# Kernel tuning notes

Hardware: AMD Instinct MI355X
Metric: run time of the kernel (lower is better)

## Reference

```python
import math
import jax, jax.numpy as jnp
import numpy as np

L, T, F = 16, 524288, 2
N_MIN, N_MAX = 16, 2048
N_POINTS = 1_048_576

# 4 bilinear corner offsets, same order as the original module
VERT_OFFSETS = jnp.asarray([[0, 0], [0, 1], [1, 0], [1, 1]], dtype=jnp.int32)


def _smallest_prime_geq(n):
    def is_prime(m):
        if m < 2:
            return False
        for p in range(2, int(m ** 0.5) + 1):
            if m % p == 0:
                return False
        return True
    while not is_prime(n):
        n += 1
    return n

PRIME = _smallest_prime_geq(2 ** 17)  # second spatial hashing prime (first is 1)


def _grid_meta():
    # per-level resolution, hashed-vs-dense flag, and offsets into the flat table
    b = math.exp((math.log(N_MAX) - math.log(N_MIN)) / (L - 1))
    resolutions, hashed, offsets = [], [], [0]
    for i in range(L):
        res = int(N_MIN * b ** i)
        n_entries = (res + 1) ** 2
        h = n_entries > T
        if h:
            n_entries = T
        resolutions.append(res)
        hashed.append(h)
        offsets.append(offsets[-1] + n_entries)
    return resolutions, hashed, offsets


def setup_inputs() -> dict:
    key = jax.random.key(0)
    k1, k2 = jax.random.split(key)
    _, _, offsets = _grid_meta()
    uv = jax.random.uniform(k1, (N_POINTS, 2), jnp.float32)  # points in [0,1)^2
    latents = jax.random.uniform(k2, (offsets[-1], F), jnp.float32, -1e-4, 1e-4)
    return {"uv": uv, "latents": latents}


def _encode(uv, latents):
    resolutions, hashed, offsets = _grid_meta()
    encs = []
    for i in range(L):  # fixed small level loop (structurally distinct per level)
        res = resolutions[i]
        uv_scaled = uv * res                                   # [N, 2]
        uv_floored = jnp.floor(uv_scaled).astype(jnp.int32)    # [N, 2]
        vert_uv = uv_floored[:, None, :] + VERT_OFFSETS        # [N, 4, 2]
        if hashed[i]:
            idx = jnp.mod(
                jnp.bitwise_xor(vert_uv[..., 0] * 1, vert_uv[..., 1] * PRIME), T
            )                                                  # [N, 4]
        else:
            idx = vert_uv[..., 0] * res + vert_uv[..., 1]      # [N, 4]
        vert_latents = latents[idx + offsets[i]]               # [N, 4, F] gather
        # bilinear lerp weights, exactly as lerp_weights in the module
        pos_offset = uv_scaled[:, None, :] - vert_uv[:, 0:1, :]          # [N, 1->4, 2]
        widths = jnp.clip(1 - VERT_OFFSETS + (2 * VERT_OFFSETS - 1) * pos_offset, 0, 1)
        w = jnp.prod(widths, axis=-1)                          # [N, 4]
        encs.append((vert_latents * w[..., None]).sum(axis=-2))  # [N, F]
    # original: stack [L,N,F] -> transpose(1,0,2) -> reshape(N, L*F) == concat on -1
    return jnp.concatenate(encs, axis=-1)                      # [N, L*F]


def reference(uv, latents):
    return _encode(uv, latents)
```

## Files before the change

### kernel.cpp

```cpp
#include <hip/hip_runtime.h>
#include <math.h>

#define NLEVELS 16
#define NDENSE 12
#define NHASH 4
#define TBITS 19
#define TMASK ((1 << TBITS) - 1)

typedef float vfloat4 __attribute__((ext_vector_type(4)));

struct Meta {
    float resf[NLEVELS];
    int   resi[NLEVELS];
    int   off[NLEVELS];
    int   prime;
};

__global__ __launch_bounds__(256, 1) void hashgrid2d_kernel(
    const float2* __restrict__ uv,
    const float2* __restrict__ lat,
    float* __restrict__ out,
    Meta m, int n)
{
    int p = blockIdx.x * blockDim.x + threadIdx.x;
    if (p >= n) return;

    float2 u = uv[p];
    const float* latf = (const float*)lat;

    float4 da[NDENSE];
    float4 db[NDENSE];
    float2 hv[NHASH][4];

#pragma unroll
    for (int i = 0; i < NDENSE; ++i) {
        float sx = u.x * m.resf[i];
        float sy = u.y * m.resf[i];
        int x0 = (int)floorf(sx);
        int y0 = (int)floorf(sy);
        int base0 = m.off[i] + x0 * m.resi[i] + y0;
        int base1 = base0 + m.resi[i];
        __builtin_memcpy(&da[i], latf + 2 * (size_t)base0, 16);
        __builtin_memcpy(&db[i], latf + 2 * (size_t)base1, 16);
    }
#pragma unroll
    for (int h = 0; h < NHASH; ++h) {
        int i = NDENSE + h;
        float sx = u.x * m.resf[i];
        float sy = u.y * m.resf[i];
        int x0 = (int)floorf(sx);
        int y0 = (int)floorf(sy);
        int yp0 = y0 * m.prime;
        int yp1 = yp0 + m.prime;
        int x1  = x0 + 1;
        const float2* tbl = lat + m.off[i];
        hv[h][0] = tbl[(x0 ^ yp0) & TMASK];
        hv[h][1] = tbl[(x0 ^ yp1) & TMASK];
        hv[h][2] = tbl[(x1 ^ yp0) & TMASK];
        hv[h][3] = tbl[(x1 ^ yp1) & TMASK];
    }

    __builtin_amdgcn_sched_barrier(0);

    float o[2 * NLEVELS];
#pragma unroll
    for (int i = 0; i < NDENSE; ++i) {
        float sx = u.x * m.resf[i];
        float sy = u.y * m.resf[i];
        float fx = floorf(sx), fy = floorf(sy);
        float px = sx - fx,   py = sy - fy;
        float w00 = (1.0f - px) * (1.0f - py);
        float w01 = (1.0f - px) * py;
        float w10 = px * (1.0f - py);
        float w11 = px * py;
        o[2*i]   = w00 * da[i].x + w01 * da[i].z + w10 * db[i].x + w11 * db[i].z;
        o[2*i+1] = w00 * da[i].y + w01 * da[i].w + w10 * db[i].y + w11 * db[i].w;
    }
#pragma unroll
    for (int h = 0; h < NHASH; ++h) {
        int i = NDENSE + h;
        float sx = u.x * m.resf[i];
        float sy = u.y * m.resf[i];
        float fx = floorf(sx), fy = floorf(sy);
        float px = sx - fx,   py = sy - fy;
        float w00 = (1.0f - px) * (1.0f - py);
        float w01 = (1.0f - px) * py;
        float w10 = px * (1.0f - py);
        float w11 = px * py;
        o[2*i]   = w00 * hv[h][0].x + w01 * hv[h][1].x + w10 * hv[h][2].x + w11 * hv[h][3].x;
        o[2*i+1] = w00 * hv[h][0].y + w01 * hv[h][1].y + w10 * hv[h][2].y + w11 * hv[h][3].y;
    }

    vfloat4* op = (vfloat4*)(out + (size_t)p * (2 * NLEVELS));
#pragma unroll
    for (int j = 0; j < 8; ++j) {
        vfloat4 w;
        w.x = o[4 * j + 0];
        w.y = o[4 * j + 1];
        w.z = o[4 * j + 2];
        w.w = o[4 * j + 3];
        op[j] = w;
    }
}

static void compute_meta(Meta& m)
{
    const double b = exp((log(2048.0) - log(16.0)) / 15.0);
    int off = 0;
    const long long T = 1LL << TBITS;
    for (int i = 0; i < NLEVELS; ++i) {
        int res = (int)(16.0 * pow(b, (double)i));
        long long n_entries = (long long)(res + 1) * (long long)(res + 1);
        if (n_entries > T) n_entries = T;
        m.resf[i] = (float)res;
        m.resi[i] = res;
        m.off[i]  = off;
        off += (int)n_entries;
    }

    int pr = 1 << 17;
    for (;;) {
        bool isp = true;
        for (long long q = 2; q * q <= pr; ++q)
            if (pr % q == 0) { isp = false; break; }
        if (isp) break;
        ++pr;
    }
    m.prime = pr;
}

extern "C" void kernel_launch(void* const* d_in, const int* in_sizes, int n_in,
                              void* d_out, int out_size, void* d_ws, size_t ws_size,
                              hipStream_t stream)
{
    const float2* uv  = (const float2*)d_in[0];
    const float2* lat = (const float2*)d_in[1];
    float* out = (float*)d_out;

    int n = in_sizes[0] / 2;

    Meta m;
    compute_meta(m);

    const int block = 256;
    const int grid = (n + block - 1) / block;
    hashgrid2d_kernel<<<grid, block, 0, stream>>>(uv, lat, out, m, n);
}
```

Measured before the change: 338.2 us.

## Split hashed levels into per-level kernels writing workspace before dense assembly

Each of the four hashed levels is now handled by its own kernel launch, which gathers that level's four corners, interpolates them, and writes a float2 per point to workspace. A final kernel gathers the dense levels, reads the four precomputed hash results, and writes the output. The aim is to keep each 4 MB hash table's random-access footprint cache-resident during its own pass instead of all four competing at once. In exchange there are extra launches, extra workspace writes and reads, and uv is re-read five times. If the workspace is too small, the original monolithic kernel is kept as a fallback.

```diff
diff --git a/kernel.cpp b/kernel.cpp
--- a/kernel.cpp
+++ b/kernel.cpp
@@ -16,9 +16,40 @@
     int   prime;
 };
 
-__global__ __launch_bounds__(256, 1) void hashgrid2d_kernel(
+__global__ void hash_level_kernel(
     const float2* __restrict__ uv,
     const float2* __restrict__ lat,
+    float2* __restrict__ ws_out,
+    float resf, int off, int prime, int n)
+{
+    int p = blockIdx.x * blockDim.x + threadIdx.x;
+    if (p >= n) return;
+    float2 u = uv[p];
+    float sx = u.x * resf, sy = u.y * resf;
+    float fx = floorf(sx), fy = floorf(sy);
+    int x0 = (int)fx, y0 = (int)fy;
+    float px = sx - fx, py = sy - fy;
+    int yp0 = y0 * prime;
+    int yp1 = yp0 + prime;
+    const float2* tb = lat + off;
+    float2 c00 = tb[(x0 ^ yp0) & TMASK];
+    float2 c01 = tb[(x0 ^ yp1) & TMASK];
+    float2 c10 = tb[((x0 + 1) ^ yp0) & TMASK];
+    float2 c11 = tb[((x0 + 1) ^ yp1) & TMASK];
+    float w00 = (1.0f - px) * (1.0f - py);
+    float w01 = (1.0f - px) * py;
+    float w10 = px * (1.0f - py);
+    float w11 = px * py;
+    float2 r;
+    r.x = w00 * c00.x + w01 * c01.x + w10 * c10.x + w11 * c11.x;
+    r.y = w00 * c00.y + w01 * c01.y + w10 * c10.y + w11 * c11.y;
+    ws_out[p] = r;
+}
+
+__global__ __launch_bounds__(256, 1) void dense_assemble_kernel(
+    const float2* __restrict__ uv,
+    const float2* __restrict__ lat,
+    const float2* __restrict__ ws,
     float* __restrict__ out,
     Meta m, int n)
 {
@@ -30,7 +61,7 @@
 
     float4 da[NDENSE];
     float4 db[NDENSE];
-    float2 hv[NHASH][4];
+    float2 hres[NHASH];
 
 #pragma unroll
     for (int i = 0; i < NDENSE; ++i) {
@@ -44,21 +75,8 @@
         __builtin_memcpy(&db[i], latf + 2 * (size_t)base1, 16);
     }
 #pragma unroll
-    for (int h = 0; h < NHASH; ++h) {
-        int i = NDENSE + h;
-        float sx = u.x * m.resf[i];
-        float sy = u.y * m.resf[i];
-        int x0 = (int)floorf(sx);
-        int y0 = (int)floorf(sy);
-        int yp0 = y0 * m.prime;
-        int yp1 = yp0 + m.prime;
-        int x1  = x0 + 1;
-        const float2* tbl = lat + m.off[i];
-        hv[h][0] = tbl[(x0 ^ yp0) & TMASK];
-        hv[h][1] = tbl[(x0 ^ yp1) & TMASK];
-        hv[h][2] = tbl[(x1 ^ yp0) & TMASK];
-        hv[h][3] = tbl[(x1 ^ yp1) & TMASK];
-    }
+    for (int h = 0; h < NHASH; ++h)
+        hres[h] = ws[(size_t)h * n + p];
 
     __builtin_amdgcn_sched_barrier(0);
 
@@ -78,7 +96,62 @@
     }
 #pragma unroll
     for (int h = 0; h < NHASH; ++h) {
+        o[2*(NDENSE+h)]   = hres[h].x;
+        o[2*(NDENSE+h)+1] = hres[h].y;
+    }
+
+    vfloat4* op = (vfloat4*)(out + (size_t)p * (2 * NLEVELS));
+#pragma unroll
+    for (int j = 0; j < 8; ++j) {
+        vfloat4 w;
+        w.x = o[4*j+0]; w.y = o[4*j+1]; w.z = o[4*j+2]; w.w = o[4*j+3];
+        op[j] = w;
+    }
+}
+
+__global__ __launch_bounds__(256, 1) void hashgrid2d_mono_kernel(
+    const float2* __restrict__ uv,
+    const float2* __restrict__ lat,
+    float* __restrict__ out,
+    Meta m, int n)
+{
+    int p = blockIdx.x * blockDim.x + threadIdx.x;
+    if (p >= n) return;
+    float2 u = uv[p];
+    const float* latf = (const float*)lat;
+    float4 da[NDENSE];
+    float4 db[NDENSE];
+    float2 hv[NHASH][4];
+#pragma unroll
+    for (int i = 0; i < NDENSE; ++i) {
+        float sx = u.x * m.resf[i];
+        float sy = u.y * m.resf[i];
+        int x0 = (int)floorf(sx);
+        int y0 = (int)floorf(sy);
+        int base0 = m.off[i] + x0 * m.resi[i] + y0;
+        int base1 = base0 + m.resi[i];
+        __builtin_memcpy(&da[i], latf + 2 * (size_t)base0, 16);
+        __builtin_memcpy(&db[i], latf + 2 * (size_t)base1, 16);
+    }
+#pragma unroll
+    for (int h = 0; h < NHASH; ++h) {
         int i = NDENSE + h;
+        float sx = u.x * m.resf[i];
+        float sy = u.y * m.resf[i];
+        int x0 = (int)floorf(sx);
+        int y0 = (int)floorf(sy);
+        int yp0 = y0 * m.prime;
+        int yp1 = yp0 + m.prime;
+        const float2* tb = lat + m.off[i];
+        hv[h][0] = tb[(x0 ^ yp0) & TMASK];
+        hv[h][1] = tb[(x0 ^ yp1) & TMASK];
+        hv[h][2] = tb[((x0+1) ^ yp0) & TMASK];
+        hv[h][3] = tb[((x0+1) ^ yp1) & TMASK];
+    }
+    __builtin_amdgcn_sched_barrier(0);
+    float o[2 * NLEVELS];
+#pragma unroll
+    for (int i = 0; i < NDENSE; ++i) {
         float sx = u.x * m.resf[i];
         float sy = u.y * m.resf[i];
         float fx = floorf(sx), fy = floorf(sy);
@@ -87,18 +160,28 @@
         float w01 = (1.0f - px) * py;
         float w10 = px * (1.0f - py);
         float w11 = px * py;
-        o[2*i]   = w00 * hv[h][0].x + w01 * hv[h][1].x + w10 * hv[h][2].x + w11 * hv[h][3].x;
-        o[2*i+1] = w00 * hv[h][0].y + w01 * hv[h][1].y + w10 * hv[h][2].y + w11 * hv[h][3].y;
-    }
-
+        o[2*i]   = w00 * da[i].x + w01 * da[i].z + w10 * db[i].x + w11 * db[i].z;
+        o[2*i+1] = w00 * da[i].y + w01 * da[i].w + w10 * db[i].y + w11 * db[i].w;
+    }
+#pragma unroll
+    for (int h = 0; h < NHASH; ++h) {
+        int i = NDENSE + h;
+        float sx = u.x * m.resf[i];
+        float sy = u.y * m.resf[i];
+        float fx = floorf(sx), fy = floorf(sy);
+        float px = sx - fx,   py = sy - fy;
+        float w00 = (1.0f - px) * (1.0f - py);
+        float w01 = (1.0f - px) * py;
+        float w10 = px * (1.0f - py);
+        float w11 = px * py;
+        o[2*i]   = w00*hv[h][0].x + w01*hv[h][1].x + w10*hv[h][2].x + w11*hv[h][3].x;
+        o[2*i+1] = w00*hv[h][0].y + w01*hv[h][1].y + w10*hv[h][2].y + w11*hv[h][3].y;
+    }
     vfloat4* op = (vfloat4*)(out + (size_t)p * (2 * NLEVELS));
 #pragma unroll
     for (int j = 0; j < 8; ++j) {
         vfloat4 w;
-        w.x = o[4 * j + 0];
-        w.y = o[4 * j + 1];
-        w.z = o[4 * j + 2];
-        w.w = o[4 * j + 3];
+        w.x = o[4*j+0]; w.y = o[4*j+1]; w.z = o[4*j+2]; w.w = o[4*j+3];
         op[j] = w;
     }
 }
@@ -117,7 +200,6 @@
         m.off[i]  = off;
         off += (int)n_entries;
     }
-
     int pr = 1 << 17;
     for (;;) {
         bool isp = true;
@@ -144,5 +226,17 @@
 
     const int block = 256;
     const int grid = (n + block - 1) / block;
-    hashgrid2d_kernel<<<grid, block, 0, stream>>>(uv, lat, out, m, n);
-}
+
+    size_t ws_needed = (size_t)NHASH * (size_t)n * sizeof(float2);
+    if (ws_size >= ws_needed) {
+        float2* wsf = (float2*)d_ws;
+        for (int h = 0; h < NHASH; ++h) {
+            int i = NDENSE + h;
+            hash_level_kernel<<<grid, block, 0, stream>>>(
+                uv, lat, wsf + (size_t)h * n, m.resf[i], m.off[i], m.prime, n);
+        }
+        dense_assemble_kernel<<<grid, block, 0, stream>>>(uv, lat, wsf, out, m, n);
+    } else {
+        hashgrid2d_mono_kernel<<<grid, block, 0, stream>>>(uv, lat, out, m, n);
+    }
+}
```

New measurement: 306.5 us. -9.4%, faster.

## Bin points spatially via counting sort to improve latent gather locality

Applied to the files above, without the earlier changes.

Adds a histogram, scan and scatter pipeline that buckets points into a 64x64 spatial grid and builds a permutation. The main kernel then processes points in binned order, so neighbouring threads gather nearby latent entries and cache reuse improves. In exchange it adds four extra launches, atomics, an indirect uv load and scattered output writes.

```diff
diff --git a/kernel.cpp b/kernel.cpp
--- a/kernel.cpp
+++ b/kernel.cpp
@@ -6,6 +6,9 @@
 #define NHASH 4
 #define TBITS 19
 #define TMASK ((1 << TBITS) - 1)
+#define BINBITS 6
+#define BINS1D (1 << BINBITS)
+#define NBINS (BINS1D * BINS1D)
 
 typedef float vfloat4 __attribute__((ext_vector_type(4)));
 
@@ -16,14 +19,76 @@
     int   prime;
 };
 
+__device__ __forceinline__ int bin_of(float2 u)
+{
+    int bu = (int)(u.x * (float)BINS1D);
+    int bv = (int)(u.y * (float)BINS1D);
+    return bv * BINS1D + bu;
+}
+
+__global__ __launch_bounds__(256) void zero_kernel(int* __restrict__ hist)
+{
+    hist[blockIdx.x * 256 + threadIdx.x] = 0;
+}
+
+__global__ __launch_bounds__(256) void hist_kernel(
+    const float2* __restrict__ uv, int n, int* __restrict__ hist)
+{
+    __shared__ int lh[NBINS];
+    for (int i = threadIdx.x; i < NBINS; i += 256) lh[i] = 0;
+    __syncthreads();
+    for (int p = blockIdx.x * 256 + threadIdx.x; p < n; p += gridDim.x * 256)
+        atomicAdd(&lh[bin_of(uv[p])], 1);
+    __syncthreads();
+    for (int i = threadIdx.x; i < NBINS; i += 256) {
+        int c = lh[i];
+        if (c) atomicAdd(&hist[i], c);
+    }
+}
+
+__global__ __launch_bounds__(256) void scan_kernel(int* __restrict__ hist)
+{
+    __shared__ int part[256];
+    int t = threadIdx.x;
+    int loc[16];
+    int s = 0;
+    int base = t * 16;
+#pragma unroll
+    for (int k = 0; k < 16; ++k) { loc[k] = hist[base + k]; s += loc[k]; }
+    part[t] = s;
+    __syncthreads();
+    for (int d = 1; d < 256; d <<= 1) {
+        int v = (t >= d) ? part[t - d] : 0;
+        __syncthreads();
+        part[t] += v;
+        __syncthreads();
+    }
+    int run = part[t] - s;
+#pragma unroll
+    for (int k = 0; k < 16; ++k) { int c = loc[k]; hist[base + k] = run; run += c; }
+}
+
+__global__ __launch_bounds__(256) void scatter_kernel(
+    const float2* __restrict__ uv, int n,
+    int* __restrict__ offs, int* __restrict__ perm)
+{
+    int p = blockIdx.x * 256 + threadIdx.x;
+    if (p >= n) return;
+    int b = bin_of(uv[p]);
+    int pos = atomicAdd(&offs[b], 1);
+    perm[pos] = p;
+}
+
 __global__ __launch_bounds__(256, 1) void hashgrid2d_kernel(
     const float2* __restrict__ uv,
     const float2* __restrict__ lat,
+    const int* __restrict__ perm,
     float* __restrict__ out,
     Meta m, int n)
 {
-    int p = blockIdx.x * blockDim.x + threadIdx.x;
-    if (p >= n) return;
+    int j = blockIdx.x * blockDim.x + threadIdx.x;
+    if (j >= n) return;
+    int p = perm ? perm[j] : j;
 
     float2 u = uv[p];
     const float* latf = (const float*)lat;
@@ -52,12 +117,11 @@
         int y0 = (int)floorf(sy);
         int yp0 = y0 * m.prime;
         int yp1 = yp0 + m.prime;
-        int x1  = x0 + 1;
-        const float2* tbl = lat + m.off[i];
-        hv[h][0] = tbl[(x0 ^ yp0) & TMASK];
-        hv[h][1] = tbl[(x0 ^ yp1) & TMASK];
-        hv[h][2] = tbl[(x1 ^ yp0) & TMASK];
-        hv[h][3] = tbl[(x1 ^ yp1) & TMASK];
+        const float2* tb = lat + m.off[i];
+        hv[h][0] = tb[(x0 ^ yp0) & TMASK];
+        hv[h][1] = tb[(x0 ^ yp1) & TMASK];
+        hv[h][2] = tb[((x0 + 1) ^ yp0) & TMASK];
+        hv[h][3] = tb[((x0 + 1) ^ yp1) & TMASK];
     }
 
     __builtin_amdgcn_sched_barrier(0);
@@ -87,19 +151,16 @@
         float w01 = (1.0f - px) * py;
         float w10 = px * (1.0f - py);
         float w11 = px * py;
-        o[2*i]   = w00 * hv[h][0].x + w01 * hv[h][1].x + w10 * hv[h][2].x + w11 * hv[h][3].x;
-        o[2*i+1] = w00 * hv[h][0].y + w01 * hv[h][1].y + w10 * hv[h][2].y + w11 * hv[h][3].y;
+        o[2*i]   = w00*hv[h][0].x + w01*hv[h][1].x + w10*hv[h][2].x + w11*hv[h][3].x;
+        o[2*i+1] = w00*hv[h][0].y + w01*hv[h][1].y + w10*hv[h][2].y + w11*hv[h][3].y;
     }
 
     vfloat4* op = (vfloat4*)(out + (size_t)p * (2 * NLEVELS));
 #pragma unroll
-    for (int j = 0; j < 8; ++j) {
+    for (int jq = 0; jq < 8; ++jq) {
         vfloat4 w;
-        w.x = o[4 * j + 0];
-        w.y = o[4 * j + 1];
-        w.z = o[4 * j + 2];
-        w.w = o[4 * j + 3];
-        op[j] = w;
+        w.x = o[4*jq+0]; w.y = o[4*jq+1]; w.z = o[4*jq+2]; w.w = o[4*jq+3];
+        op[jq] = w;
     }
 }
 
@@ -117,7 +178,6 @@
         m.off[i]  = off;
         off += (int)n_entries;
     }
-
     int pr = 1 << 17;
     for (;;) {
         bool isp = true;
@@ -144,5 +204,17 @@
 
     const int block = 256;
     const int grid = (n + block - 1) / block;
-    hashgrid2d_kernel<<<grid, block, 0, stream>>>(uv, lat, out, m, n);
-}
+
+    size_t ws_needed = (size_t)NBINS * 4 + (size_t)n * 4;
+    if (ws_size >= ws_needed) {
+        int* hist = (int*)d_ws;
+        int* perm = (int*)d_ws + NBINS;
+        zero_kernel<<<NBINS / 256, 256, 0, stream>>>(hist);
+        hist_kernel<<<64, 256, 0, stream>>>(uv, n, hist);
+        scan_kernel<<<1, 256, 0, stream>>>(hist);
+        scatter_kernel<<<grid, block, 0, stream>>>(uv, n, hist, perm);
+        hashgrid2d_kernel<<<grid, block, 0, stream>>>(uv, lat, perm, out, m, n);
+    } else {
+        hashgrid2d_kernel<<<grid, block, 0, stream>>>(uv, lat, nullptr, out, m, n);
+    }
+}
```

Result: faster. 320.4 us (-5.3%).

## Bin points spatially before encoding to improve gather locality

Applied to the files above, without the earlier changes.

Adds a pre-pass that buckets points into a 128x128 spatial grid of fixed-capacity bins using atomics, then encodes points bin by bin so neighbouring threads gather nearby latent entries. Points that overflow a bin go to a separate overflow kernel. The aim is better cache hit rates for the random table gathers. In exchange it adds extra launches, atomic scatter traffic, scattered output writes and a workspace requirement. If the workspace is too small it falls back to the original single kernel.

```diff
diff --git a/kernel.cpp b/kernel.cpp
--- a/kernel.cpp
+++ b/kernel.cpp
@@ -6,6 +6,10 @@
 #define NHASH 4
 #define TBITS 19
 #define TMASK ((1 << TBITS) - 1)
+#define BINBITS 7
+#define BINS1D (1 << BINBITS)
+#define NBINS (BINS1D * BINS1D)
+#define CAP 128
 
 typedef float vfloat4 __attribute__((ext_vector_type(4)));
 
@@ -16,18 +20,20 @@
     int   prime;
 };
 
-__global__ __launch_bounds__(256, 1) void hashgrid2d_kernel(
-    const float2* __restrict__ uv,
-    const float2* __restrict__ lat,
-    float* __restrict__ out,
-    Meta m, int n)
-{
-    int p = blockIdx.x * blockDim.x + threadIdx.x;
-    if (p >= n) return;
-
-    float2 u = uv[p];
+__device__ __forceinline__ int bin_of(float2 u)
+{
+    int bu = (int)(u.x * (float)BINS1D);
+    int bv = (int)(u.y * (float)BINS1D);
+    return bv * BINS1D + bu;
+}
+
+__device__ __forceinline__ void encode_point(
+    float2 u, int p,
+    const float2* __restrict__ lat,
+    float* __restrict__ out,
+    const Meta& m)
+{
     const float* latf = (const float*)lat;
-
     float4 da[NDENSE];
     float4 db[NDENSE];
     float2 hv[NHASH][4];
@@ -52,12 +58,11 @@
         int y0 = (int)floorf(sy);
         int yp0 = y0 * m.prime;
         int yp1 = yp0 + m.prime;
-        int x1  = x0 + 1;
-        const float2* tbl = lat + m.off[i];
-        hv[h][0] = tbl[(x0 ^ yp0) & TMASK];
-        hv[h][1] = tbl[(x0 ^ yp1) & TMASK];
-        hv[h][2] = tbl[(x1 ^ yp0) & TMASK];
-        hv[h][3] = tbl[(x1 ^ yp1) & TMASK];
+        const float2* tb = lat + m.off[i];
+        hv[h][0] = tb[(x0 ^ yp0) & TMASK];
+        hv[h][1] = tb[(x0 ^ yp1) & TMASK];
+        hv[h][2] = tb[((x0 + 1) ^ yp0) & TMASK];
+        hv[h][3] = tb[((x0 + 1) ^ yp1) & TMASK];
     }
 
     __builtin_amdgcn_sched_barrier(0);
@@ -87,20 +92,86 @@
         float w01 = (1.0f - px) * py;
         float w10 = px * (1.0f - py);
         float w11 = px * py;
-        o[2*i]   = w00 * hv[h][0].x + w01 * hv[h][1].x + w10 * hv[h][2].x + w11 * hv[h][3].x;
-        o[2*i+1] = w00 * hv[h][0].y + w01 * hv[h][1].y + w10 * hv[h][2].y + w11 * hv[h][3].y;
+        o[2*i]   = w00*hv[h][0].x + w01*hv[h][1].x + w10*hv[h][2].x + w11*hv[h][3].x;
+        o[2*i+1] = w00*hv[h][0].y + w01*hv[h][1].y + w10*hv[h][2].y + w11*hv[h][3].y;
     }
 
     vfloat4* op = (vfloat4*)(out + (size_t)p * (2 * NLEVELS));
 #pragma unroll
-    for (int j = 0; j < 8; ++j) {
+    for (int jq = 0; jq < 8; ++jq) {
         vfloat4 w;
-        w.x = o[4 * j + 0];
-        w.y = o[4 * j + 1];
-        w.z = o[4 * j + 2];
-        w.w = o[4 * j + 3];
-        op[j] = w;
-    }
+        w.x = o[4*jq+0]; w.y = o[4*jq+1]; w.z = o[4*jq+2]; w.w = o[4*jq+3];
+        op[jq] = w;
+    }
+}
+
+__global__ __launch_bounds__(256) void zero_kernel(int* __restrict__ cnt, int total)
+{
+    int i = blockIdx.x * 256 + threadIdx.x;
+    if (i < total) cnt[i] = 0;
+}
+
+__global__ __launch_bounds__(256) void scatter_kernel(
+    const float2* __restrict__ uv, int n,
+    int* __restrict__ cnt, int* __restrict__ ocnt,
+    float2* __restrict__ slotUV, int* __restrict__ slotIdx,
+    int* __restrict__ overflow)
+{
+    int p = blockIdx.x * 256 + threadIdx.x;
+    if (p >= n) return;
+    float2 u = uv[p];
+    int b = bin_of(u);
+    int s = atomicAdd(&cnt[b], 1);
+    if (s < CAP) {
+        slotUV[b * CAP + s]  = u;
+        slotIdx[b * CAP + s] = p;
+    } else {
+        int o = atomicAdd(ocnt, 1);
+        overflow[o] = p;
+    }
+}
+
+__global__ __launch_bounds__(256, 1) void hashgrid2d_main(
+    const float2* __restrict__ lat,
+    const int* __restrict__ cnt,
+    const float2* __restrict__ slotUV,
+    const int* __restrict__ slotIdx,
+    float* __restrict__ out,
+    Meta m)
+{
+    int b = blockIdx.x * 2 + (threadIdx.x >> 7);
+    int s = threadIdx.x & (CAP - 1);
+    int c = cnt[b];
+    if (s >= c) return;
+    float2 u = slotUV[b * CAP + s];
+    int p = slotIdx[b * CAP + s];
+    encode_point(u, p, lat, out, m);
+}
+
+__global__ __launch_bounds__(256) void overflow_kernel(
+    const float2* __restrict__ uv,
+    const float2* __restrict__ lat,
+    const int* __restrict__ ocnt,
+    const int* __restrict__ overflow,
+    float* __restrict__ out,
+    Meta m)
+{
+    int tot = *ocnt;
+    for (int j = blockIdx.x * 256 + threadIdx.x; j < tot; j += gridDim.x * 256) {
+        int p = overflow[j];
+        encode_point(uv[p], p, lat, out, m);
+    }
+}
+
+__global__ __launch_bounds__(256, 1) void hashgrid2d_mono(
+    const float2* __restrict__ uv,
+    const float2* __restrict__ lat,
+    float* __restrict__ out,
+    Meta m, int n)
+{
+    int p = blockIdx.x * blockDim.x + threadIdx.x;
+    if (p >= n) return;
+    encode_point(uv[p], p, lat, out, m);
 }
 
 static void compute_meta(Meta& m)
@@ -117,7 +188,6 @@
         m.off[i]  = off;
         off += (int)n_entries;
     }
-
     int pr = 1 << 17;
     for (;;) {
         bool isp = true;
@@ -142,7 +212,28 @@
     Meta m;
     compute_meta(m);
 
+    const size_t cnt_ints   = 16640;
+    const size_t uv_bytes   = (size_t)NBINS * CAP * sizeof(float2);
+    const size_t idx_bytes  = (size_t)NBINS * CAP * sizeof(int);
+    const size_t ws_needed  = cnt_ints * 4 + uv_bytes + idx_bytes + (size_t)n * 4;
+
     const int block = 256;
     const int grid = (n + block - 1) / block;
-    hashgrid2d_kernel<<<grid, block, 0, stream>>>(uv, lat, out, m, n);
-}
+
+    if (ws_size >= ws_needed) {
+        int*    cnt      = (int*)d_ws;
+        int*    ocnt     = cnt + NBINS;
+        float2* slotUV   = (float2*)((char*)d_ws + cnt_ints * 4);
+        int*    slotIdx  = (int*)((char*)slotUV + uv_bytes);
+        int*    overflow = (int*)((char*)slotIdx + idx_bytes);
+
+        zero_kernel<<<(NBINS + 1 + 255) / 256, 256, 0, stream>>>(cnt, NBINS + 1);
+        scatter_kernel<<<grid, block, 0, stream>>>(uv, n, cnt, ocnt,
+                                                   slotUV, slotIdx, overflow);
+        hashgrid2d_main<<<NBINS / 2, 256, 0, stream>>>(lat, cnt, slotUV,
+                                                       slotIdx, out, m);
+        overflow_kernel<<<64, 256, 0, stream>>>(uv, lat, ocnt, overflow, out, m);
+    } else {
+        hashgrid2d_mono<<<grid, block, 0, stream>>>(uv, lat, out, m, n);
+    }
+}
```

After: 277.8 us. 1.22x faster.
